# Kernel tuning notes

Hardware: AMD Instinct MI355X
Metric: run time of the kernel (lower is better)

## Reference

```python
import jax, jax.numpy as jnp
import numpy as np

BN_EPS = 1e-5

def mish(x):
    return x * jnp.tanh(jax.nn.softplus(x))

def setup_inputs() -> dict:
    key = jax.random.key(0)
    k1, k2, k3 = jax.random.split(key, 3)
    B, C, D, N = 16, 512, 512, 2048
    x = jax.random.normal(k1, (B, C, N), dtype=jnp.float32)
    W = jax.random.normal(k2, (D, C), dtype=jnp.float32) * (1.0 / np.sqrt(C))
    gamma = jnp.ones((D,), dtype=jnp.float32)
    bn_beta = jnp.zeros((D,), dtype=jnp.float32)
    beta = jax.random.normal(k3, (1,), dtype=jnp.float32) * 0.1
    return {"x": x, "W": W, "gamma": gamma, "bn_beta": bn_beta, "beta": beta}

def reference(x, W, gamma, bn_beta, beta):
    # 1x1 conv: [B,C,N] -> [B,D,N]
    q = jnp.einsum('dc,bcn->bdn', W, x)
    # BatchNorm1d (training-mode batch stats, biased variance) over (B, N) per channel
    mean = jnp.mean(q, axis=(0, 2), keepdims=True)
    var = jnp.mean(jnp.square(q - mean), axis=(0, 2), keepdims=True)
    q = (q - mean) * jax.lax.rsqrt(var + BN_EPS)
    q = q * gamma[None, :, None] + bn_beta[None, :, None]
    h = mish(q)                                   # proj_key  [B,D,N]; proj_query = h^T [B,N,D]
    energy = jnp.einsum('bdn,bdm->bnm', h, h)     # bmm(Q, Q^T) -> [B,N,N]
    attn = jax.nn.softmax(energy, axis=-1)
    out_x = jnp.einsum('bdm,bnm->bdn', h, attn)   # bmm(proj_key, attn^T)
    return beta[0] * out_x + h
```

## Files before the change

kernel.cpp:

```cpp
#include <hip/hip_runtime.h>
#include <cstdint>
#include <cstddef>

#define B_DIM 16
#define C_DIM 512
#define D_DIM 512
#define N_DIM 2048

typedef _Float16 half8  __attribute__((ext_vector_type(8)));
typedef _Float16 half4v __attribute__((ext_vector_type(4)));
typedef float    floatx4 __attribute__((ext_vector_type(4)));

__device__ __forceinline__ void gload_lds16(const _Float16* g, _Float16* l)
{
    __builtin_amdgcn_global_load_lds((const __attribute__((address_space(1))) void*)g,
                                     (__attribute__((address_space(3))) void*)l,
                                     16, 0, 0);
}

template<int EPI, int TRI, typename OutT>
__global__ __launch_bounds__(256, 2)
void gemm_nt(const _Float16* __restrict__ A, size_t strideA,
             const _Float16* __restrict__ Bm, size_t strideB,
             OutT* __restrict__ Cm, size_t strideC,
             int M, int Ncols, int K,
             const float* __restrict__ beta_ptr,
             const _Float16* __restrict__ Hm, size_t strideH)
{
    constexpr int BK  = 64;
    constexpr int TP  = 136;
    __shared__ _Float16 smem[128 * TP];
    _Float16* sA = smem;
    _Float16* sB = smem + 128 * BK;

    const int gx = gridDim.x, gy = gridDim.y;
    const int nwg = gx * gy * gridDim.z;
    int flat = blockIdx.x + gx * (blockIdx.y + gy * blockIdx.z);
    const int q8 = nwg >> 3;
    flat = (flat & 7) * q8 + (flat >> 3);

    int bx, by, bz;
    if (TRI) {
        int tri = flat % gx;
        bz = flat / gx;
        const int nt = Ncols >> 7;
        int r = 0;
        while (tri >= nt - r) { tri -= nt - r; ++r; }
        bx = r; by = r + tri;
    } else {
        bx = flat % gx;
        by = (flat / gx) % gy;
        bz = flat / (gx * gy);
    }

    const _Float16* Ab = A  + (size_t)bz * strideA;
    const _Float16* Bb = Bm + (size_t)bz * strideB;

    const int m0 = bx * 128;
    const int n0 = by * 128;

    const int tid  = threadIdx.x;
    const int lane = tid & 63;
    const int wv   = tid >> 6;
    const int wr   = (tid >> 7) & 1;
    const int wc   = (tid >> 6) & 1;
    const int fr   = lane & 15;
    const int hi   = lane >> 4;

    const int srow = tid >> 3;
    const int sk   = ((tid & 7) ^ (srow & 7)) * 8;

    const _Float16* gA0 = Ab + (size_t)(m0 + srow) * K + sk;
    const _Float16* gB0 = Bb + (size_t)(n0 + srow) * K + sk;
    _Float16* lA = &sA[(wv * 8) * BK];
    _Float16* lB = &sB[(wv * 8) * BK];

    const int ch0 = ((0 * 4 + hi) ^ (fr & 7)) * 8;
    const int ch1 = ((1 * 4 + hi) ^ (fr & 7)) * 8;
    const _Float16* fA = &sA[(wr * 64 + fr) * BK];
    const _Float16* fB = &sB[(wc * 64 + fr) * BK];

    floatx4 acc[4][4] = {};

    for (int k0 = 0; k0 < K; k0 += BK) {
        __syncthreads();
        #pragma unroll
        for (int p = 0; p < 4; ++p) {
            gload_lds16(gA0 + (size_t)(p * 32) * K + k0, lA + p * 32 * BK);
            gload_lds16(gB0 + (size_t)(p * 32) * K + k0, lB + p * 32 * BK);
        }
        __syncthreads();
        #pragma unroll
        for (int sub = 0; sub < 2; ++sub) {
            const int ch = (sub == 0) ? ch0 : ch1;
            half8 af[4], bf[4];
            #pragma unroll
            for (int i = 0; i < 4; ++i) af[i] = *(const half8*)(fA + i * 16 * BK + ch);
            #pragma unroll
            for (int j = 0; j < 4; ++j) bf[j] = *(const half8*)(fB + j * 16 * BK + ch);
            #pragma unroll
            for (int i = 0; i < 4; ++i)
                #pragma unroll
                for (int j = 0; j < 4; ++j)
                    acc[i][j] = __builtin_amdgcn_mfma_f32_16x16x32_f16(af[i], bf[j], acc[i][j], 0, 0, 0);
        }
    }

    float beta = 0.0f;
    const _Float16* Hb = nullptr;
    if (EPI == 1) { beta = beta_ptr[0]; Hb = Hm + (size_t)bz * strideH; }
    OutT* Cb = Cm + (size_t)bz * strideC;

    const bool mirror = TRI && (bx != by);
    if (mirror) __syncthreads();

    #pragma unroll
    for (int i = 0; i < 4; ++i) {
        const int rowb = m0 + wr * 64 + i * 16 + (hi << 2);
        #pragma unroll
        for (int j = 0; j < 4; ++j) {
            const int col = n0 + wc * 64 + j * 16 + fr;
            half4v mv;
            #pragma unroll
            for (int r = 0; r < 4; ++r) {
                size_t idx = (size_t)(rowb + r) * Ncols + col;
                float v = acc[i][j][r];
                if (EPI == 1) v = beta * v + (float)Hb[idx];
                Cb[idx] = (OutT)v;
                if (TRI) mv[r] = (_Float16)v;
            }
            if (mirror) {
                const int cl = wc * 64 + j * 16 + fr;
                const int rl = wr * 64 + i * 16 + (hi << 2);
                *(half4v*)(smem + cl * TP + rl) = mv;
            }
        }
    }

    if (mirror) {
        __syncthreads();
        #pragma unroll
        for (int k = 0; k < 8; ++k) {
            const int fl = tid + 256 * k;
            const int rr = fl >> 4;
            const int cc = (fl & 15) * 8;
            half8 v = *(const half8*)(smem + rr * TP + cc);
            *(half8*)((_Float16*)(void*)Cb + (size_t)(n0 + rr) * Ncols + m0 + cc) = v;
        }
    }
}

__global__ void convert_w_kernel(const float* __restrict__ W, _Float16* __restrict__ Wh, int n)
{
    int i = blockIdx.x * 256 + threadIdx.x;
    if (i < n) Wh[i] = (_Float16)W[i];
}

__global__ void transpose_convert_x(const float* __restrict__ x, _Float16* __restrict__ xT)
{
    __shared__ float tile[32][33];
    const int bz = blockIdx.z;
    const int n0 = blockIdx.x * 32;
    const int c0 = blockIdx.y * 32;
    const int tx = threadIdx.x, ty = threadIdx.y;
    const float* xb = x + (size_t)bz * C_DIM * N_DIM;
    #pragma unroll
    for (int j = 0; j < 4; ++j)
        tile[ty + j * 8][tx] = xb[(size_t)(c0 + ty + j * 8) * N_DIM + n0 + tx];
    __syncthreads();
    _Float16* xtb = xT + (size_t)bz * N_DIM * C_DIM;
    #pragma unroll
    for (int j = 0; j < 4; ++j)
        xtb[(size_t)(n0 + ty + j * 8) * C_DIM + c0 + tx] = (_Float16)tile[tx][ty + j * 8];
}

__global__ __launch_bounds__(256)
void bn_stats(const _Float16* __restrict__ q, const float* __restrict__ gamma,
              const float* __restrict__ bn_beta, float2* __restrict__ stats)
{
    const int d = blockIdx.x;
    const int tid = threadIdx.x;
    float s = 0.f, ss = 0.f;
    for (int b = 0; b < B_DIM; ++b) {
        const _Float16* row = q + ((size_t)b * D_DIM + d) * N_DIM;
        half8 v = *(const half8*)(row + tid * 8);
        #pragma unroll
        for (int j = 0; j < 8; ++j) {
            float f = (float)v[j];
            s += f; ss += f * f;
        }
    }
    #pragma unroll
    for (int off = 32; off; off >>= 1) {
        s  += __shfl_down(s,  off, 64);
        ss += __shfl_down(ss, off, 64);
    }
    __shared__ float red[8];
    const int wv = tid >> 6;
    if ((tid & 63) == 0) { red[wv] = s; red[4 + wv] = ss; }
    __syncthreads();
    if (tid == 0) {
        s  = red[0] + red[1] + red[2] + red[3];
        ss = red[4] + red[5] + red[6] + red[7];
        const float inv = 1.0f / (float)(B_DIM * N_DIM);
        float mean = s * inv;
        float var  = ss * inv - mean * mean;
        float scale = gamma[d] * rsqrtf(var + 1e-5f);
        stats[d] = make_float2(scale, bn_beta[d] - mean * scale);
    }
}

__device__ __forceinline__ float mishf(float v)
{
    float t = __expf(fminf(v, 30.0f));
    float u = 1.0f + t;
    u *= u;
    return v * (u - 1.0f) * __builtin_amdgcn_rcpf(u + 1.0f);
}

__global__ void bn_mish(const _Float16* __restrict__ q, const float2* __restrict__ stats,
                        _Float16* __restrict__ h, _Float16* __restrict__ hT)
{
    __shared__ float tile[32][33];
    const int bz = blockIdx.z;
    const int n0 = blockIdx.x * 32;
    const int d0 = blockIdx.y * 32;
    const int tx = threadIdx.x, ty = threadIdx.y;
    const _Float16* qb = q + (size_t)bz * D_DIM * N_DIM;
    _Float16* hb = h + (size_t)bz * D_DIM * N_DIM;
    #pragma unroll
    for (int j = 0; j < 4; ++j) {
        int d = d0 + ty + j * 8;
        float2 sc = stats[d];
        float v  = (float)qb[(size_t)d * N_DIM + n0 + tx];
        float hv = mishf(v * sc.x + sc.y);
        tile[ty + j * 8][tx] = hv;
        hb[(size_t)d * N_DIM + n0 + tx] = (_Float16)hv;
    }
    __syncthreads();
    _Float16* htb = hT + (size_t)bz * N_DIM * D_DIM;
    #pragma unroll
    for (int j = 0; j < 4; ++j)
        htb[(size_t)(n0 + ty + j * 8) * D_DIM + d0 + tx] = (_Float16)tile[tx][ty + j * 8];
}

__global__ __launch_bounds__(256)
void softmax_rows(const _Float16* __restrict__ energy, size_t strideE,
                  _Float16* __restrict__ attn, size_t strideAt)
{
    const int wid  = threadIdx.x >> 6;
    const int lane = threadIdx.x & 63;
    const int n = blockIdx.x * 4 + wid;
    const int b = blockIdx.y;
    const _Float16* row = energy + (size_t)b * strideE + (size_t)n * N_DIM;
    _Float16*      orow = attn   + (size_t)b * strideAt + (size_t)n * N_DIM;
    float f[32];
    #pragma unroll
    for (int w = 0; w < 4; ++w) {
        half8 v = *(const half8*)(row + w * 512 + lane * 8);
        #pragma unroll
        for (int j = 0; j < 8; ++j) f[w * 8 + j] = (float)v[j];
    }
    float mx = f[0];
    #pragma unroll
    for (int k = 1; k < 32; ++k) mx = fmaxf(mx, f[k]);
    #pragma unroll
    for (int off = 1; off < 64; off <<= 1) mx = fmaxf(mx, __shfl_xor(mx, off, 64));
    float s = 0.f;
    #pragma unroll
    for (int k = 0; k < 32; ++k) { f[k] = __expf(f[k] - mx); s += f[k]; }
    #pragma unroll
    for (int off = 1; off < 64; off <<= 1) s += __shfl_xor(s, off, 64);
    const float inv = 1.0f / s;
    #pragma unroll
    for (int w = 0; w < 4; ++w) {
        half8 o;
        #pragma unroll
        for (int j = 0; j < 8; ++j) o[j] = (_Float16)(f[w * 8 + j] * inv);
        *(half8*)(orow + w * 512 + lane * 8) = o;
    }
}

extern "C" void kernel_launch(void* const* d_in, const int* in_sizes, int n_in,
                              void* d_out, int out_size, void* d_ws, size_t ws_size,
                              hipStream_t stream)
{
    const float* x       = (const float*)d_in[0];
    const float* W       = (const float*)d_in[1];
    const float* gamma   = (const float*)d_in[2];
    const float* bn_beta = (const float*)d_in[3];
    const float* beta    = (const float*)d_in[4];
    float* out = (float*)d_out;

    char* ws = (char*)d_ws;
    size_t off = 0;
    auto take = [&](size_t bytes) -> char* {
        char* p = ws + off;
        off = (off + bytes + 255) & ~(size_t)255;
        return p;
    };

    _Float16* xT    = (_Float16*)take((size_t)B_DIM * N_DIM * C_DIM * 2);
    _Float16* q     = (_Float16*)take((size_t)B_DIM * D_DIM * N_DIM * 2);
    _Float16* h     = (_Float16*)take((size_t)B_DIM * D_DIM * N_DIM * 2);
    _Float16* Wh    = (_Float16*)take((size_t)D_DIM * C_DIM * 2);
    float2*   stats = (float2*)  take((size_t)D_DIM * sizeof(float2));
    _Float16* hT    = xT;

    const size_t eSz = (size_t)N_DIM * N_DIM * 2;
    const size_t fixedEnd = off;
    const int full = (ws_size >= fixedEnd + (size_t)B_DIM * eSz + 1024) ? 1 : 0;
    _Float16* energy = (_Float16*)take(full ? (size_t)B_DIM * eSz : eSz);
    _Float16* attn   = energy;

    const int NT = N_DIM / 128;
    const int TRI_BLOCKS = NT * (NT + 1) / 2;

    convert_w_kernel<<<dim3((D_DIM * C_DIM + 255) / 256), dim3(256), 0, stream>>>(W, Wh, D_DIM * C_DIM);
    transpose_convert_x<<<dim3(N_DIM / 32, C_DIM / 32, B_DIM), dim3(32, 8), 0, stream>>>(x, xT);
    gemm_nt<0, 0, _Float16><<<dim3(D_DIM / 128, N_DIM / 128, B_DIM), dim3(256), 0, stream>>>(
        Wh, 0, xT, (size_t)N_DIM * C_DIM, q, (size_t)D_DIM * N_DIM,
        D_DIM, N_DIM, C_DIM, nullptr, nullptr, 0);
    bn_stats<<<dim3(D_DIM), dim3(256), 0, stream>>>(q, gamma, bn_beta, stats);
    bn_mish<<<dim3(N_DIM / 32, D_DIM / 32, B_DIM), dim3(32, 8), 0, stream>>>(q, stats, h, hT);

    if (full) {
        gemm_nt<0, 1, _Float16><<<dim3(TRI_BLOCKS, 1, B_DIM), dim3(256), 0, stream>>>(
            hT, (size_t)N_DIM * D_DIM, hT, (size_t)N_DIM * D_DIM, energy, (size_t)N_DIM * N_DIM,
            N_DIM, N_DIM, D_DIM, nullptr, nullptr, 0);
        softmax_rows<<<dim3(N_DIM / 4, B_DIM), dim3(256), 0, stream>>>(
            energy, (size_t)N_DIM * N_DIM, attn, (size_t)N_DIM * N_DIM);
        gemm_nt<1, 0, float><<<dim3(D_DIM / 128, N_DIM / 128, B_DIM), dim3(256), 0, stream>>>(
            h, (size_t)D_DIM * N_DIM, attn, (size_t)N_DIM * N_DIM, out, (size_t)D_DIM * N_DIM,
            D_DIM, N_DIM, N_DIM, beta, h, (size_t)D_DIM * N_DIM);
    } else {
        for (int b = 0; b < B_DIM; ++b) {
            const _Float16* hTb = hT + (size_t)b * N_DIM * D_DIM;
            const _Float16* hb  = h  + (size_t)b * D_DIM * N_DIM;
            gemm_nt<0, 1, _Float16><<<dim3(TRI_BLOCKS, 1, 1), dim3(256), 0, stream>>>(
                hTb, 0, hTb, 0, energy, 0, N_DIM, N_DIM, D_DIM, nullptr, nullptr, 0);
            softmax_rows<<<dim3(N_DIM / 4, 1), dim3(256), 0, stream>>>(energy, 0, attn, 0);
            gemm_nt<1, 0, float><<<dim3(D_DIM / 128, N_DIM / 128, 1), dim3(256), 0, stream>>>(
                hb, 0, attn, 0, out + (size_t)b * D_DIM * N_DIM, 0,
                D_DIM, N_DIM, N_DIM, beta, hb, 0);
        }
    }
}
```

Baseline: 234.3 us.

## Fuse x transpose-convert into projection GEMM and compute BN partial stats in epilogue

The projection GEMM now reads fp32 x directly, converting it to fp16 and staging it transposed into LDS, so the separate transpose_convert_x kernel and its xT buffer are gone. The same GEMM epilogue reduces per-channel sums and squared sums from the fp32 accumulators into per-tile slots, and a small bn_finalize kernel replaces the full-read bn_stats pass. This removes two memory passes over large tensors. In exchange the B-tile load becomes strided scalar fp32 global reads done in registers rather than async global-to-LDS loads, which may slow the GEMM main loop. hT now has its own allocation instead of aliasing xT.

```diff
diff --git a/kernel.cpp b/kernel.cpp
--- a/kernel.cpp
+++ b/kernel.cpp
@@ -18,14 +18,16 @@
                                      16, 0, 0);
 }
 
-template<int EPI, int TRI, typename OutT>
+template<int EPI, int TRI, int TRANSB, typename OutT>
 __global__ __launch_bounds__(256, 2)
 void gemm_nt(const _Float16* __restrict__ A, size_t strideA,
              const _Float16* __restrict__ Bm, size_t strideB,
+             const float* __restrict__ Bf, size_t strideBf, int ldBf,
              OutT* __restrict__ Cm, size_t strideC,
              int M, int Ncols, int K,
              const float* __restrict__ beta_ptr,
-             const _Float16* __restrict__ Hm, size_t strideH)
+             const _Float16* __restrict__ Hm, size_t strideH,
+             float* __restrict__ st_s, float* __restrict__ st_ss)
 {
     constexpr int BK  = 64;
     constexpr int TP  = 136;
@@ -53,8 +55,7 @@
         bz = flat / (gx * gy);
     }
 
-    const _Float16* Ab = A  + (size_t)bz * strideA;
-    const _Float16* Bb = Bm + (size_t)bz * strideB;
+    const _Float16* Ab = A + (size_t)bz * strideA;
 
     const int m0 = bx * 128;
     const int n0 = by * 128;
@@ -71,7 +72,13 @@
     const int sk   = ((tid & 7) ^ (srow & 7)) * 8;
 
     const _Float16* gA0 = Ab + (size_t)(m0 + srow) * K + sk;
-    const _Float16* gB0 = Bb + (size_t)(n0 + srow) * K + sk;
+    const _Float16* gB0 = nullptr;
+    const float*    xB  = nullptr;
+    if (TRANSB) {
+        xB = Bf + (size_t)bz * strideBf + n0;
+    } else {
+        gB0 = Bm + (size_t)bz * strideB + (size_t)(n0 + srow) * K + sk;
+    }
     _Float16* lA = &sA[(wv * 8) * BK];
     _Float16* lB = &sB[(wv * 8) * BK];
 
@@ -85,9 +92,23 @@
     for (int k0 = 0; k0 < K; k0 += BK) {
         __syncthreads();
         #pragma unroll
-        for (int p = 0; p < 4; ++p) {
+        for (int p = 0; p < 4; ++p)
             gload_lds16(gA0 + (size_t)(p * 32) * K + k0, lA + p * 32 * BK);
-            gload_lds16(gB0 + (size_t)(p * 32) * K + k0, lB + p * 32 * BK);
+        if (TRANSB) {
+            const int cch = (tid >> 5) * 8;
+            #pragma unroll
+            for (int j = 0; j < 4; ++j) {
+                const int n = (tid & 31) + 32 * j;
+                half8 hv;
+                #pragma unroll
+                for (int i = 0; i < 8; ++i)
+                    hv[i] = (_Float16)xB[(size_t)(k0 + cch + i) * ldBf + n];
+                *(half8*)(&sB[n * BK + (((cch >> 3) ^ (n & 7)) * 8)]) = hv;
+            }
+        } else {
+            #pragma unroll
+            for (int p = 0; p < 4; ++p)
+                gload_lds16(gB0 + (size_t)(p * 32) * K + k0, lB + p * 32 * BK);
         }
         __syncthreads();
         #pragma unroll
@@ -148,6 +169,32 @@
             *(half8*)((_Float16*)(void*)Cb + (size_t)(n0 + rr) * Ncols + m0 + cc) = v;
         }
     }
+
+    if (EPI == 2) {
+        #pragma unroll
+        for (int i = 0; i < 4; ++i) {
+            #pragma unroll
+            for (int r = 0; r < 4; ++r) {
+                float s = 0.f, ss2 = 0.f;
+                #pragma unroll
+                for (int j = 0; j < 4; ++j) {
+                    float v = acc[i][j][r];
+                    s += v; ss2 += v * v;
+                }
+                #pragma unroll
+                for (int o = 1; o < 16; o <<= 1) {
+                    s   += __shfl_xor(s,   o, 64);
+                    ss2 += __shfl_xor(ss2, o, 64);
+                }
+                if (fr == 0) {
+                    const int d = m0 + wr * 64 + i * 16 + (hi << 2) + r;
+                    const size_t slot = (((size_t)bz * gy + by) * 2 + wc) * M + d;
+                    st_s[slot]  = s;
+                    st_ss[slot] = ss2;
+                }
+            }
+        }
+    }
 }
 
 __global__ void convert_w_kernel(const float* __restrict__ W, _Float16* __restrict__ Wh, int n)
@@ -156,58 +203,22 @@
     if (i < n) Wh[i] = (_Float16)W[i];
 }
 
-__global__ void transpose_convert_x(const float* __restrict__ x, _Float16* __restrict__ xT)
-{
-    __shared__ float tile[32][33];
-    const int bz = blockIdx.z;
-    const int n0 = blockIdx.x * 32;
-    const int c0 = blockIdx.y * 32;
-    const int tx = threadIdx.x, ty = threadIdx.y;
-    const float* xb = x + (size_t)bz * C_DIM * N_DIM;
-    #pragma unroll
-    for (int j = 0; j < 4; ++j)
-        tile[ty + j * 8][tx] = xb[(size_t)(c0 + ty + j * 8) * N_DIM + n0 + tx];
-    __syncthreads();
-    _Float16* xtb = xT + (size_t)bz * N_DIM * C_DIM;
-    #pragma unroll
-    for (int j = 0; j < 4; ++j)
-        xtb[(size_t)(n0 + ty + j * 8) * C_DIM + c0 + tx] = (_Float16)tile[tx][ty + j * 8];
-}
-
-__global__ __launch_bounds__(256)
-void bn_stats(const _Float16* __restrict__ q, const float* __restrict__ gamma,
-              const float* __restrict__ bn_beta, float2* __restrict__ stats)
-{
-    const int d = blockIdx.x;
-    const int tid = threadIdx.x;
+__global__ void bn_finalize(const float* __restrict__ st_s, const float* __restrict__ st_ss,
+                            const float* __restrict__ gamma, const float* __restrict__ bn_beta,
+                            float2* __restrict__ stats, int nslots)
+{
+    int d = blockIdx.x * 256 + threadIdx.x;
+    if (d >= D_DIM) return;
     float s = 0.f, ss = 0.f;
-    for (int b = 0; b < B_DIM; ++b) {
-        const _Float16* row = q + ((size_t)b * D_DIM + d) * N_DIM;
-        half8 v = *(const half8*)(row + tid * 8);
-        #pragma unroll
-        for (int j = 0; j < 8; ++j) {
-            float f = (float)v[j];
-            s += f; ss += f * f;
-        }
-    }
-    #pragma unroll
-    for (int off = 32; off; off >>= 1) {
-        s  += __shfl_down(s,  off, 64);
-        ss += __shfl_down(ss, off, 64);
-    }
-    __shared__ float red[8];
-    const int wv = tid >> 6;
-    if ((tid & 63) == 0) { red[wv] = s; red[4 + wv] = ss; }
-    __syncthreads();
-    if (tid == 0) {
-        s  = red[0] + red[1] + red[2] + red[3];
-        ss = red[4] + red[5] + red[6] + red[7];
-        const float inv = 1.0f / (float)(B_DIM * N_DIM);
-        float mean = s * inv;
-        float var  = ss * inv - mean * mean;
-        float scale = gamma[d] * rsqrtf(var + 1e-5f);
-        stats[d] = make_float2(scale, bn_beta[d] - mean * scale);
-    }
+    for (int p = 0; p < nslots; ++p) {
+        s  += st_s[(size_t)p * D_DIM + d];
+        ss += st_ss[(size_t)p * D_DIM + d];
+    }
+    const float inv = 1.0f / (float)(B_DIM * N_DIM);
+    float mean = s * inv;
+    float var  = ss * inv - mean * mean;
+    float scale = gamma[d] * rsqrtf(var + 1e-5f);
+    stats[d] = make_float2(scale, bn_beta[d] - mean * scale);
 }
 
 __device__ __forceinline__ float mishf(float v)
@@ -300,12 +311,14 @@
         return p;
     };
 
-    _Float16* xT    = (_Float16*)take((size_t)B_DIM * N_DIM * C_DIM * 2);
+    _Float16* hT    = (_Float16*)take((size_t)B_DIM * N_DIM * D_DIM * 2);
     _Float16* q     = (_Float16*)take((size_t)B_DIM * D_DIM * N_DIM * 2);
     _Float16* h     = (_Float16*)take((size_t)B_DIM * D_DIM * N_DIM * 2);
     _Float16* Wh    = (_Float16*)take((size_t)D_DIM * C_DIM * 2);
     float2*   stats = (float2*)  take((size_t)D_DIM * sizeof(float2));
-    _Float16* hT    = xT;
+    const int NSLOT = B_DIM * (N_DIM / 128) * 2;
+    float*    st_s  = (float*)   take((size_t)NSLOT * D_DIM * 4);
+    float*    st_ss = (float*)   take((size_t)NSLOT * D_DIM * 4);
 
     const size_t eSz = (size_t)N_DIM * N_DIM * 2;
     const size_t fixedEnd = off;
@@ -317,32 +330,35 @@
     const int TRI_BLOCKS = NT * (NT + 1) / 2;
 
     convert_w_kernel<<<dim3((D_DIM * C_DIM + 255) / 256), dim3(256), 0, stream>>>(W, Wh, D_DIM * C_DIM);
-    transpose_convert_x<<<dim3(N_DIM / 32, C_DIM / 32, B_DIM), dim3(32, 8), 0, stream>>>(x, xT);
-    gemm_nt<0, 0, _Float16><<<dim3(D_DIM / 128, N_DIM / 128, B_DIM), dim3(256), 0, stream>>>(
-        Wh, 0, xT, (size_t)N_DIM * C_DIM, q, (size_t)D_DIM * N_DIM,
-        D_DIM, N_DIM, C_DIM, nullptr, nullptr, 0);
-    bn_stats<<<dim3(D_DIM), dim3(256), 0, stream>>>(q, gamma, bn_beta, stats);
+    gemm_nt<2, 0, 1, _Float16><<<dim3(D_DIM / 128, N_DIM / 128, B_DIM), dim3(256), 0, stream>>>(
+        Wh, 0, nullptr, 0, x, (size_t)C_DIM * N_DIM, N_DIM,
+        q, (size_t)D_DIM * N_DIM, D_DIM, N_DIM, C_DIM,
+        nullptr, nullptr, 0, st_s, st_ss);
+    bn_finalize<<<dim3((D_DIM + 255) / 256), dim3(256), 0, stream>>>(st_s, st_ss, gamma, bn_beta, stats, NSLOT);
     bn_mish<<<dim3(N_DIM / 32, D_DIM / 32, B_DIM), dim3(32, 8), 0, stream>>>(q, stats, h, hT);
 
     if (full) {
-        gemm_nt<0, 1, _Float16><<<dim3(TRI_BLOCKS, 1, B_DIM), dim3(256), 0, stream>>>(
-            hT, (size_t)N_DIM * D_DIM, hT, (size_t)N_DIM * D_DIM, energy, (size_t)N_DIM * N_DIM,
-            N_DIM, N_DIM, D_DIM, nullptr, nullptr, 0);
+        gemm_nt<0, 1, 0, _Float16><<<dim3(TRI_BLOCKS, 1, B_DIM), dim3(256), 0, stream>>>(
+            hT, (size_t)N_DIM * D_DIM, hT, (size_t)N_DIM * D_DIM, nullptr, 0, 0,
+            energy, (size_t)N_DIM * N_DIM, N_DIM, N_DIM, D_DIM,
+            nullptr, nullptr, 0, nullptr, nullptr);
         softmax_rows<<<dim3(N_DIM / 4, B_DIM), dim3(256), 0, stream>>>(
             energy, (size_t)N_DIM * N_DIM, attn, (size_t)N_DIM * N_DIM);
-        gemm_nt<1, 0, float><<<dim3(D_DIM / 128, N_DIM / 128, B_DIM), dim3(256), 0, stream>>>(
-            h, (size_t)D_DIM * N_DIM, attn, (size_t)N_DIM * N_DIM, out, (size_t)D_DIM * N_DIM,
-            D_DIM, N_DIM, N_DIM, beta, h, (size_t)D_DIM * N_DIM);
+        gemm_nt<1, 0, 0, float><<<dim3(D_DIM / 128, N_DIM / 128, B_DIM), dim3(256), 0, stream>>>(
+            h, (size_t)D_DIM * N_DIM, attn, (size_t)N_DIM * N_DIM, nullptr, 0, 0,
+            out, (size_t)D_DIM * N_DIM, D_DIM, N_DIM, N_DIM,
+            beta, h, (size_t)D_DIM * N_DIM, nullptr, nullptr);
     } else {
         for (int b = 0; b < B_DIM; ++b) {
             const _Float16* hTb = hT + (size_t)b * N_DIM * D_DIM;
             const _Float16* hb  = h  + (size_t)b * D_DIM * N_DIM;
-            gemm_nt<0, 1, _Float16><<<dim3(TRI_BLOCKS, 1, 1), dim3(256), 0, stream>>>(
-                hTb, 0, hTb, 0, energy, 0, N_DIM, N_DIM, D_DIM, nullptr, nullptr, 0);
+            gemm_nt<0, 1, 0, _Float16><<<dim3(TRI_BLOCKS, 1, 1), dim3(256), 0, stream>>>(
+                hTb, 0, hTb, 0, nullptr, 0, 0, energy, 0, N_DIM, N_DIM, D_DIM,
+                nullptr, nullptr, 0, nullptr, nullptr);
             softmax_rows<<<dim3(N_DIM / 4, 1), dim3(256), 0, stream>>>(energy, 0, attn, 0);
-            gemm_nt<1, 0, float><<<dim3(D_DIM / 128, N_DIM / 128, 1), dim3(256), 0, stream>>>(
-                hb, 0, attn, 0, out + (size_t)b * D_DIM * N_DIM, 0,
-                D_DIM, N_DIM, N_DIM, beta, hb, 0);
-        }
-    }
-}
+            gemm_nt<1, 0, 0, float><<<dim3(D_DIM / 128, N_DIM / 128, 1), dim3(256), 0, stream>>>(
+                hb, 0, attn, 0, nullptr, 0, 0, out + (size_t)b * D_DIM * N_DIM, 0,
+                D_DIM, N_DIM, N_DIM, beta, hb, 0, nullptr, nullptr);
+        }
+    }
+}
```

New measurement: 370.8 us. 58.2% more time.
